# Performance work log

Hardware: AMD Instinct MI355X
Metric: run time of the kernel (lower is better)

The kernel has to match this reference:

```python
import jax, jax.numpy as jnp
import numpy as np

B, NO, NR, DIM, RNN = 64, 128, 512, 1024, 1000


def setup_inputs() -> dict:
    key = jax.random.key(0)
    ks = jax.random.split(key, 32)
    def rn(k, shape, s=0.02):
        return jax.random.normal(k, shape, dtype=jnp.float32) * s
    inp = {}
    inp['obj_labels'] = jax.random.randint(ks[0], (B, NO, 1), 0, 26)
    inp['obj_masks'] = jnp.ones((B, NO), jnp.float32)
    inp['rela_masks'] = jnp.ones((B, NR), jnp.float32)
    inp['rela_edges'] = jax.random.randint(ks[1], (B, NR, 2), 0, NO)
    inp['rela_feats'] = jax.random.normal(ks[2], (B, NR, 8), dtype=jnp.float32)
    inp['box_feats'] = jax.random.normal(ks[3], (B, NO, 5), dtype=jnp.float32)
    # parameters
    inp['emb_table'] = jax.random.uniform(ks[4], (26, 128), jnp.float32, -0.1, 0.1)
    inp['w_objfeat'] = rn(ks[5], (5, 128));        inp['b_objfeat'] = jnp.zeros((128,), jnp.float32)
    inp['w_cat'] = rn(ks[6], (256, 128));          inp['b_cat'] = jnp.zeros((128,), jnp.float32)
    inp['w_obj'] = rn(ks[7], (128, RNN));          inp['b_obj'] = jnp.zeros((RNN,), jnp.float32)
    inp['w_rela'] = rn(ks[8], (8, RNN));           inp['b_rela'] = jnp.zeros((RNN,), jnp.float32)
    inp['w_gnn'] = rn(ks[9], (3 * RNN, RNN));      inp['b_gnn'] = jnp.zeros((RNN,), jnp.float32)
    inp['w_att_obj'] = rn(ks[10], (RNN, 1));       inp['b_att_obj'] = jnp.zeros((1,), jnp.float32)
    inp['w_att_rela'] = rn(ks[11], (RNN, 1));      inp['b_att_rela'] = jnp.zeros((1,), jnp.float32)
    inp['w_read'] = rn(ks[12], (2 * RNN, DIM));    inp['b_read'] = jnp.zeros((DIM,), jnp.float32)
    inp['w_fc'] = rn(ks[13], (DIM, 32 * 14 * 6));  inp['b_fc'] = jnp.zeros((32 * 14 * 6,), jnp.float32)
    inp['wt1'] = rn(ks[14], (32, 25, 3, 3));       inp['bt1'] = jnp.zeros((25,), jnp.float32)
    inp['wt2'] = rn(ks[15], (25, 25, 3, 3));       inp['bt2'] = jnp.zeros((25,), jnp.float32)
    inp['wt3'] = rn(ks[16], (25, 25, 3, 3));       inp['bt3'] = jnp.zeros((25,), jnp.float32)
    inp['wt4'] = rn(ks[17], (25, 25, 3, 3));       inp['bt4'] = jnp.zeros((25,), jnp.float32)
    return inp


def _attn(feats, mask, w, b):
    # feats: (B, N, RNN); mask: (B, N)
    dot = (jnp.tanh(feats) @ w + b)[..., 0]              # (B, N)
    wgt = jax.nn.softmax(dot, axis=1) * mask
    wgt = wgt / jnp.sum(wgt, axis=1, keepdims=True)
    return jnp.einsum('bn,bnd->bd', wgt, feats)          # (B, RNN)


def _up2(x):
    return jnp.repeat(jnp.repeat(x, 2, axis=2), 2, axis=3)


def _convT(x, w, b):
    # torch ConvTranspose2d (stride=1, pad=0) == full-padded corr with flipped kernel
    k = jnp.transpose(w, (1, 0, 2, 3))[:, :, ::-1, ::-1]  # (out, in, 3, 3)
    y = jax.lax.conv_general_dilated(x, k, (1, 1), [(2, 2), (2, 2)],
                                     dimension_numbers=('NCHW', 'OIHW', 'NCHW'))
    return y + b[None, :, None, None]


def reference(obj_labels, obj_masks, rela_masks, rela_edges, rela_feats, box_feats,
              emb_table, w_objfeat, b_objfeat, w_cat, b_cat, w_obj, b_obj,
              w_rela, b_rela, w_gnn, b_gnn, w_att_obj, b_att_obj,
              w_att_rela, b_att_rela, w_read, b_read, w_fc, b_fc,
              wt1, bt1, wt2, bt2, wt3, bt3, wt4, bt4):
    relu = jax.nn.relu
    # embeddings (dropout = identity at inference)
    obj_embed = relu(emb_table[obj_labels])[:, :, 0, :]                   # (B, NO, 128)
    obj_f = relu(box_feats @ w_objfeat + b_objfeat)                       # (B, NO, 128)
    obj_embed = relu(jnp.concatenate([obj_f, obj_embed], -1) @ w_cat + b_cat)
    obj_vecs = relu(obj_embed @ w_obj + b_obj)                            # (B, NO, 1000)
    rela_vecs = relu(rela_feats @ w_rela + b_rela)                        # (B, NR, 1000)
    # GNN: gather endpoints, concat, linear+relu, mask
    s = jnp.take_along_axis(obj_vecs, rela_edges[:, :, 0:1], axis=1)      # (B, NR, 1000)
    o = jnp.take_along_axis(obj_vecs, rela_edges[:, :, 1:2], axis=1)
    t = jnp.concatenate([s, rela_vecs, o], axis=-1)                       # (B, NR, 3000)
    new_rela = relu(t @ w_gnn + b_gnn) * rela_masks[..., None]
    # attention pooling
    a_obj = _attn(obj_vecs, obj_masks, w_att_obj, b_att_obj)
    a_rel = _attn(new_rela, rela_masks, w_att_rela, b_att_rela)
    enc = relu(jnp.concatenate([a_obj, a_rel], axis=1) @ w_read + b_read)  # (B, DIM)
    # decoder
    x = (enc @ w_fc + b_fc).reshape(-1, 32, 14, 6)
    x = relu(_convT(_up2(x), wt1, bt1))
    x = relu(_convT(_up2(x), wt2, bt2))
    x = relu(_convT(_up2(x), wt3, bt3))
    x = relu(_convT(_up2(x), wt4, bt4))
    x = jax.nn.sigmoid(x)                                                  # (B, 25, 254, 126)
    return enc, x
```

## Files before the change

### kernel.cpp

```cpp
#include <hip/hip_runtime.h>
#include <hip/hip_bf16.h>
#include <hip/hip_fp16.h>

#define B_    64
#define NO_   128
#define NR_   512
#define RNN_  1000
#define DIM_  1024

typedef short short8 __attribute__((ext_vector_type(8)));
typedef float f32x4  __attribute__((ext_vector_type(4)));
typedef float f32x2v __attribute__((ext_vector_type(2)));
typedef float f32x4v __attribute__((ext_vector_type(4)));

static __device__ __forceinline__ float bf2f(unsigned short u) {
    union { unsigned int i; float f; } x; x.i = ((unsigned int)u) << 16; return x.f;
}
static __device__ __forceinline__ short f2bf_s(float f) {
    __hip_bfloat16 h = __float2bfloat16(f);
    return *reinterpret_cast<short*>(&h);
}

#define GLOAD_LDS16(gp, lp) \
    __builtin_amdgcn_global_load_lds((const __attribute__((address_space(1))) void*)(gp), \
                                     (__attribute__((address_space(3))) void*)(lp), 16, 0, 0)

__global__ void k_obj_embed(const int* __restrict__ labels,
                            const float* __restrict__ box_feats,
                            const float* __restrict__ emb_table,
                            const float* __restrict__ w_objfeat, const float* __restrict__ b_objfeat,
                            const float* __restrict__ w_cat, const float* __restrict__ b_cat,
                            __hip_bfloat16* __restrict__ out)
{
    const int row = blockIdx.x;
    const int tid = threadIdx.x;
    __shared__ __align__(16) float cat[256];
    __shared__ float bf[5];
    if (tid < 5) bf[tid] = box_feats[row * 5 + tid];
    __syncthreads();
    float acc = b_objfeat[tid];
#pragma unroll
    for (int k = 0; k < 5; ++k) acc += bf[k] * w_objfeat[k * 128 + tid];
    cat[tid] = fmaxf(acc, 0.f);
    const int label = labels[row];
    cat[128 + tid] = fmaxf(emb_table[label * 128 + tid], 0.f);
    __syncthreads();
    float acc2 = b_cat[tid];
#pragma unroll 4
    for (int k4 = 0; k4 < 64; ++k4) {
        const f32x4 c4 = *(const f32x4*)&cat[k4 * 4];
        acc2 += c4[0] * w_cat[(k4 * 4 + 0) * 128 + tid];
        acc2 += c4[1] * w_cat[(k4 * 4 + 1) * 128 + tid];
        acc2 += c4[2] * w_cat[(k4 * 4 + 2) * 128 + tid];
        acc2 += c4[3] * w_cat[(k4 * 4 + 3) * 128 + tid];
    }
    out[(size_t)row * 128 + tid] = __float2bfloat16(fmaxf(acc2, 0.f));
}

__global__ void k_transpose(const float* __restrict__ W, __hip_bfloat16* __restrict__ Wt,
                            int K, int N, int ldn, int Kpad)
{
    __shared__ float t[32][33];
    const int k0 = blockIdx.x * 32, n0 = blockIdx.y * 32;
    const int c = threadIdx.x & 31, r8 = threadIdx.x >> 5;
#pragma unroll
    for (int rr = r8; rr < 32; rr += 8) {
        int k = k0 + rr, n = n0 + c;
        t[rr][c] = (k < K && n < N) ? W[(size_t)k * ldn + n] : 0.f;
    }
    __syncthreads();
#pragma unroll
    for (int rr = r8; rr < 32; rr += 8)
        Wt[(size_t)(n0 + rr) * Kpad + k0 + c] = __float2bfloat16(t[c][rr]);
}

__global__ void k_weff(const float* __restrict__ w, float* __restrict__ wg, int IC, int OC)
{
    const int idx = blockIdx.x * 256 + threadIdx.x;
    if (idx >= IC * OC) return;
    const float* wp = w + (size_t)idx * 9;
    float wl[9];
#pragma unroll
    for (int k = 0; k < 9; ++k) wl[k] = wp[k];
    const float rm_[2][2][3] = {{{0.f,1.f,1.f},{1.f,0.f,0.f}},
                                {{0.f,0.f,1.f},{1.f,1.f,0.f}}};
    float* o = wg + (size_t)idx * 16;
#pragma unroll
    for (int py = 0; py < 2; ++py)
#pragma unroll
    for (int px = 0; px < 2; ++px)
#pragma unroll
    for (int r = 0; r < 2; ++r)
#pragma unroll
    for (int c = 0; c < 2; ++c) {
        float s = 0.f;
#pragma unroll
        for (int ky = 0; ky < 3; ++ky)
#pragma unroll
        for (int kx = 0; kx < 3; ++kx)
            s += rm_[py][r][ky] * rm_[px][c][kx] * wl[ky * 3 + kx];
        o[(r * 2 + c) * 4 + (py * 2 + px)] = s;
    }
}

__global__ void k_zero_border(float* __restrict__ buf, int PH, int PW, int IR0, int IR1, int IC0, int IC1)
{
    float* plane = buf + (size_t)blockIdx.x * PH * PW;
    const int tid = threadIdx.x;
    const int topN = IR0 * PW;
    for (int i = tid; i < topN; i += 256) plane[i] = 0.f;
    const int botBase = IR1 * PW, botN = (PH - IR1) * PW;
    for (int i = tid; i < botN; i += 256) plane[botBase + i] = 0.f;
    const int rows = IR1 - IR0;
    const int wL = IC0, wR = PW - IC1, wLR = wL + wR;
    const int n = rows * wLR;
    for (int i = tid; i < n; i += 256) {
        const int r = i / wLR, c = i - r * wLR;
        const int col = (c < wL) ? c : (IC1 + c - wL);
        plane[(IR0 + r) * PW + col] = 0.f;
    }
}

__global__ void k_rv(const float* __restrict__ rela_feats, const float* __restrict__ w_rela,
                     const float* __restrict__ b_rela, __hip_bfloat16* __restrict__ rv)
{
    const int tid = threadIdx.x;
    const int r0 = blockIdx.x * 16;
    __shared__ float rf[16][8];
    if (tid < 128) rf[tid >> 3][tid & 7] = rela_feats[(size_t)(r0 + (tid >> 3)) * 8 + (tid & 7)];
    __syncthreads();
    const int row = r0 + (tid >> 4);
    const int cg = (tid & 15) * 64;
    float rloc[8];
#pragma unroll
    for (int f = 0; f < 8; ++f) rloc[f] = rf[tid >> 4][f];
    __hip_bfloat16* orow = rv + (size_t)row * 1024;
#pragma unroll
    for (int ch = 0; ch < 8; ++ch) {
        const int c = cg + ch * 8;
        float a[8];
        if (c < RNN_) {
            const float4 b0 = *(const float4*)(b_rela + c);
            const float4 b1 = *(const float4*)(b_rela + c + 4);
            a[0] = b0.x; a[1] = b0.y; a[2] = b0.z; a[3] = b0.w;
            a[4] = b1.x; a[5] = b1.y; a[6] = b1.z; a[7] = b1.w;
#pragma unroll
            for (int f = 0; f < 8; ++f) {
                const float4 w0 = *(const float4*)(w_rela + f * RNN_ + c);
                const float4 w1 = *(const float4*)(w_rela + f * RNN_ + c + 4);
                const float rfv = rloc[f];
                a[0] += rfv * w0.x; a[1] += rfv * w0.y; a[2] += rfv * w0.z; a[3] += rfv * w0.w;
                a[4] += rfv * w1.x; a[5] += rfv * w1.y; a[6] += rfv * w1.z; a[7] += rfv * w1.w;
            }
#pragma unroll
            for (int j = 0; j < 8; ++j) a[j] = fmaxf(a[j], 0.f);
        } else {
#pragma unroll
            for (int j = 0; j < 8; ++j) a[j] = 0.f;
        }
        short8 pk;
#pragma unroll
        for (int j = 0; j < 8; ++j) pk[j] = f2bf_s(a[j]);
        *(short8*)(orow + c) = pk;
    }
}

template<int MODE>
__global__ __launch_bounds__(256)
void mfma_gemm(const __hip_bfloat16* __restrict__ A, const __hip_bfloat16* __restrict__ Bt, int Kpad,
               const float* __restrict__ bias, int ldc, int ncols,
               __hip_bfloat16* __restrict__ outB,
               const __half* __restrict__ P13H, const int* __restrict__ edges,
               const float* __restrict__ masks)
{
    __shared__ __align__(16) ushort smem[8704];
    ushort* lA = smem;
    ushort* lB = smem + 4096;
    const int tid = threadIdx.x;
    const int l = (blockIdx.x & 7) * ((int)gridDim.x >> 3) + ((int)blockIdx.x >> 3);
    const int n0 = (l & 7) * 128;
    const int m0 = (l >> 3) * 128;
    const int wave = tid >> 6, lane = tid & 63;
    const int wr = wave >> 1, wc = wave & 1;
    const int lr = lane >> 4, lc = lane & 15;
    const int lrow = lane >> 2;
    const int lcol = (lane & 3) * 8;
    f32x4 acc[4][4];
#pragma unroll
    for (int i = 0; i < 4; ++i)
#pragma unroll
        for (int j = 0; j < 4; ++j) acc[i][j] = (f32x4){0.f, 0.f, 0.f, 0.f};

    for (int k0 = 0; k0 < Kpad; k0 += 32) {
        __syncthreads();
#pragma unroll
        for (int j = 0; j < 2; ++j) {
            const int rbase = j * 64 + wave * 16;
            GLOAD_LDS16(A  + (size_t)(m0 + rbase + lrow) * Kpad + k0 + lcol, &lA[rbase * 32]);
            GLOAD_LDS16(Bt + (size_t)(n0 + rbase + lrow) * Kpad + k0 + lcol, &lB[rbase * 32]);
        }
        __syncthreads();
        short8 af[4], bfr[4];
#pragma unroll
        for (int mi = 0; mi < 4; ++mi)
            af[mi] = *(const short8*)&lA[(wr * 64 + mi * 16 + lc) * 32 + lr * 8];
#pragma unroll
        for (int ni = 0; ni < 4; ++ni)
            bfr[ni] = *(const short8*)&lB[(wc * 64 + ni * 16 + lc) * 32 + lr * 8];
#pragma unroll
        for (int mi = 0; mi < 4; ++mi)
#pragma unroll
            for (int ni = 0; ni < 4; ++ni)
                acc[mi][ni] = __builtin_amdgcn_mfma_f32_16x16x32_bf16(af[mi], bfr[ni], acc[mi][ni], 0, 0, 0);
    }

    float* ftile = (float*)smem;
    const int erow = tid >> 3;
    const int ecol0 = (tid & 7) * 16;
#pragma unroll
    for (int mi = 0; mi < 4; ++mi) {
        __syncthreads();
#pragma unroll
        for (int ni = 0; ni < 4; ++ni) {
            const int colL = wc * 64 + ni * 16 + lc;
#pragma unroll
            for (int r = 0; r < 4; ++r)
                ftile[(wr * 16 + lr * 4 + r) * 136 + colL] = acc[mi][ni][r];
        }
        __syncthreads();
        const int rowL = (erow < 16) ? (mi * 16 + erow) : (64 + mi * 16 + (erow - 16));
        const int grow = m0 + rowL;
        const int gcol = n0 + ecol0;
        float v[16];
#pragma unroll
        for (int j = 0; j < 4; ++j) {
            const f32x4 t4 = *(const f32x4*)&ftile[erow * 136 + ecol0 + j * 4];
            v[j*4+0] = t4[0]; v[j*4+1] = t4[1]; v[j*4+2] = t4[2]; v[j*4+3] = t4[3];
        }
        if (MODE == 0) {
            short8 pk0, pk1;
#pragma unroll
            for (int j = 0; j < 16; ++j) {
                const int c = gcol + j;
                const float bb = (c < ncols) ? bias[c] : 0.f;
                const short s = f2bf_s(fmaxf(v[j] + bb, 0.f));
                if (j < 8) pk0[j] = s; else pk1[j - 8] = s;
            }
            *(short8*)(outB + (size_t)grow * 1024 + gcol)     = pk0;
            *(short8*)(outB + (size_t)grow * 1024 + gcol + 8) = pk1;
        } else if (MODE == 1) {
            __half* outH = (__half*)outB;
            if (gcol + 15 < ncols) {
                __half h[16];
#pragma unroll
                for (int j = 0; j < 16; ++j) h[j] = __float2half(v[j]);
                *(short8*)(outH + (size_t)grow * ldc + gcol)     = *(short8*)&h[0];
                *(short8*)(outH + (size_t)grow * ldc + gcol + 8) = *(short8*)&h[8];
            } else {
#pragma unroll
                for (int j = 0; j < 16; ++j) {
                    const int c = gcol + j;
                    if (c < ncols) outH[(size_t)grow * ldc + c] = __float2half(v[j]);
                }
            }
        } else {
            const int b = grow >> 9;
            const int e0 = edges[grow * 2], e1 = edges[grow * 2 + 1];
            const float mk = masks[grow];
            const __half* p0 = P13H + (size_t)(b * NO_ + e0) * 2000 + gcol;
            const __half* p1 = P13H + (size_t)(b * NO_ + e1) * 2000 + RNN_ + gcol;
            if (gcol + 15 < ncols) {
                __half h0[16], h1[16];
                *(short8*)&h0[0] = *(const short8*)p0;  *(short8*)&h0[8] = *(const short8*)(p0 + 8);
                *(short8*)&h1[0] = *(const short8*)p1;  *(short8*)&h1[8] = *(const short8*)(p1 + 8);
                float bb[16];
#pragma unroll
                for (int j = 0; j < 4; ++j) {
                    const float4 b4 = *(const float4*)(bias + gcol + j * 4);
                    bb[j*4+0] = b4.x; bb[j*4+1] = b4.y; bb[j*4+2] = b4.z; bb[j*4+3] = b4.w;
                }
                short8 pk0, pk1;
#pragma unroll
                for (int j = 0; j < 16; ++j) {
                    float val = v[j] + bb[j] + __half2float(h0[j]) + __half2float(h1[j]);
                    const short s = f2bf_s(fmaxf(val, 0.f) * mk);
                    if (j < 8) pk0[j] = s; else pk1[j - 8] = s;
                }
                *(short8*)(outB + (size_t)grow * RNN_ + gcol)     = pk0;
                *(short8*)(outB + (size_t)grow * RNN_ + gcol + 8) = pk1;
            } else if (gcol < ncols) {
#pragma unroll
                for (int j = 0; j < 16; ++j) {
                    const int c = gcol + j;
                    if (c < ncols) {
                        float val = v[j] + bias[c] + __half2float(p0[j]) + __half2float(p1[j]);
                        outB[(size_t)grow * RNN_ + c] = __float2bfloat16(fmaxf(val, 0.f) * mk);
                    }
                }
            }
        }
    }
}

__global__ void k_gemm_sk(const float* __restrict__ A, const float* __restrict__ W,
                          float* __restrict__ part, int N, int K, int ldw, int Kc)
{
    __shared__ float As[16][68];
    __shared__ float Ws[16][68];
    const int tid = threadIdx.x;
    const int n0 = blockIdx.x * 64;
    const int kz = blockIdx.y;
    const int kstart = kz * Kc;
    const int kend = (kstart + Kc < K) ? (kstart + Kc) : K;
    const int ty = tid >> 4, tx = tid & 15;
    float acc[4][4] = {};
    for (int k0 = kstart; k0 < kend; k0 += 16) {
#pragma unroll
        for (int i = 0; i < 4; ++i) {
            int lin = i * 256 + tid;
            int r = lin >> 4, kk = lin & 15;
            int k = k0 + kk;
            As[kk][r] = (k < kend) ? A[(size_t)r * K + k] : 0.f;
            int kr = lin >> 6, c = lin & 63;
            int kw = k0 + kr, cc = n0 + c;
            Ws[kr][c] = (kw < kend && cc < N) ? W[(size_t)kw * ldw + cc] : 0.f;
        }
        __syncthreads();
#pragma unroll
        for (int kk = 0; kk < 16; ++kk) {
            const float4 av = *reinterpret_cast<const float4*>(&As[kk][ty * 4]);
            const float4 wv = *reinterpret_cast<const float4*>(&Ws[kk][tx * 4]);
            const float a4[4] = {av.x, av.y, av.z, av.w};
            const float w4[4] = {wv.x, wv.y, wv.z, wv.w};
#pragma unroll
            for (int i = 0; i < 4; ++i)
#pragma unroll
                for (int j = 0; j < 4; ++j) acc[i][j] += a4[i] * w4[j];
        }
        __syncthreads();
    }
#pragma unroll
    for (int i = 0; i < 4; ++i) {
        const int row = ty * 4 + i;
#pragma unroll
        for (int j = 0; j < 4; ++j) {
            const int col = n0 + tx * 4 + j;
            if (col < N)
                part[((size_t)kz * 64 + row) * N + col] = acc[i][j];
        }
    }
}

__global__ void k_sk_reduce(const float* __restrict__ part, const float* __restrict__ bias,
                            float* __restrict__ out, int N, int KS, int ldo, int act)
{
    const int idx = blockIdx.x * 256 + threadIdx.x;
    if (idx >= 64 * N) return;
    const int row = idx / N, col = idx - row * N;
    float s = bias[col];
    for (int z = 0; z < KS; ++z) s += part[((size_t)z * 64 + row) * N + col];
    if (act) s = fmaxf(s, 0.f);
    out[(size_t)row * ldo + col] = s;
}

__global__ void k_att_dot(const __hip_bfloat16* __restrict__ feats, const float* __restrict__ w_att,
                          const float* __restrict__ b_att, float* __restrict__ dot, int D, int ld)
{
    const int row = blockIdx.x;
    const int tid = threadIdx.x;
    const int c = tid * 4;
    float s = 0.f;
    if (c < D) {
        const ushort4 v = *(const ushort4*)(feats + (size_t)row * ld + c);
        const float4 wv = *(const float4*)(w_att + c);
        s  = tanhf(bf2f(v.x)) * wv.x;
        s += tanhf(bf2f(v.y)) * wv.y;
        s += tanhf(bf2f(v.z)) * wv.z;
        s += tanhf(bf2f(v.w)) * wv.w;
    }
#pragma unroll
    for (int o = 32; o > 0; o >>= 1) s += __shfl_down(s, o, 64);
    __shared__ float part[4];
    if ((tid & 63) == 0) part[tid >> 6] = s;
    __syncthreads();
    if (tid == 0) dot[row] = part[0] + part[1] + part[2] + part[3] + b_att[0];
}

__global__ void k_softmax(const float* __restrict__ dot, const float* __restrict__ mask,
                          float* __restrict__ wgt, int Nn)
{
    const int b = blockIdx.x, tid = threadIdx.x;
    __shared__ float red[512];
    float v = dot[b * Nn + tid];
    red[tid] = v; __syncthreads();
    for (int s = Nn >> 1; s > 0; s >>= 1) { if (tid < s) red[tid] = fmaxf(red[tid], red[tid + s]); __syncthreads(); }
    float mx = red[0]; __syncthreads();
    float e = expf(v - mx);
    red[tid] = e; __syncthreads();
    for (int s = Nn >> 1; s > 0; s >>= 1) { if (tid < s) red[tid] += red[tid + s]; __syncthreads(); }
    float sm = red[0]; __syncthreads();
    float w0 = (e / sm) * mask[b * Nn + tid];
    red[tid] = w0; __syncthreads();
    for (int s = Nn >> 1; s > 0; s >>= 1) { if (tid < s) red[tid] += red[tid + s]; __syncthreads(); }
    wgt[b * Nn + tid] = w0 / red[0];
}

__global__ void k_wsum(const __hip_bfloat16* __restrict__ feats, const float* __restrict__ wgt,
                       float* __restrict__ out, int Nn, int D, int ld, int ldo, int off)
{
    const int b = blockIdx.x;
    const int tid = threadIdx.x;
    __shared__ float wl[512];
    for (int i = tid; i < Nn; i += 256) wl[i] = wgt[b * Nn + i];
    __syncthreads();
    const int d0 = tid * 4;
    if (d0 >= D) return;
    float a0 = 0.f, a1 = 0.f, a2 = 0.f, a3 = 0.f;
    const __hip_bfloat16* fp = feats + (size_t)b * Nn * ld + d0;
#pragma unroll 8
    for (int n = 0; n < Nn; ++n) {
        const ushort4 v = *(const ushort4*)(fp + (size_t)n * ld);
        const float w = wl[n];
        a0 += w * bf2f(v.x); a1 += w * bf2f(v.y);
        a2 += w * bf2f(v.z); a3 += w * bf2f(v.w);
    }
    *(float4*)(out + (size_t)b * ldo + off + d0) = make_float4(a0, a1, a2, a3);
}

__global__ void k_convt5(const float* __restrict__ src, const float* __restrict__ wg,
                         const float* __restrict__ bias, float* __restrict__ dst,
                         int IC, int OC, int SH, int SW, int act,
                         int dro, int dco, int DPH, int DPW)
{
    const int QH = SH + 1, QW = SW + 1;
    const int ocg = blockIdx.y, b = blockIdx.z;
    const int tid = threadIdx.x;
    const int p = blockIdx.x * blockDim.x + tid;
    if (p >= QH * QW) return;
    const int a = p / QW, g = p % QW;
    const bool rm = (a > 0), rp = (a < SH);
    const bool cm = (g > 0), cp = (g < SW);
    f32x2v acc2[5][2];
#pragma unroll
    for (int ol = 0; ol < 5; ++ol) { acc2[ol][0] = (f32x2v){0.f, 0.f}; acc2[ol][1] = (f32x2v){0.f, 0.f}; }
    const float* sb = src + (size_t)(b * IC) * SH * SW;
    const int base = (a - 1) * SW + (g - 1);
    for (int ic = 0; ic < IC; ++ic) {
        const float* s = sb + (size_t)ic * SH * SW;
        const float s00 = (rm && cm) ? s[base] : 0.f;
        const float s01 = (rm && cp) ? s[base + 1] : 0.f;
        const float s10 = (rp && cm) ? s[base + SW] : 0.f;
        const float s11 = (rp && cp) ? s[base + SW + 1] : 0.f;
        const f32x2v b0 = {s00, s00}, b1 = {s01, s01}, b2 = {s10, s10}, b3 = {s11, s11};
        const float* wf = wg + ((size_t)ic * OC + ocg * 5) * 16;
#pragma unroll
        for (int ol = 0; ol < 5; ++ol) {
            const f32x4v w0 = *(const f32x4v*)(wf + ol * 16 + 0);
            const f32x4v w1 = *(const f32x4v*)(wf + ol * 16 + 4);
            const f32x4v w2 = *(const f32x4v*)(wf + ol * 16 + 8);
            const f32x4v w3 = *(const f32x4v*)(wf + ol * 16 + 12);
            acc2[ol][0] += b0 * __builtin_shufflevector(w0, w0, 0, 1);
            acc2[ol][0] += b1 * __builtin_shufflevector(w1, w1, 0, 1);
            acc2[ol][0] += b2 * __builtin_shufflevector(w2, w2, 0, 1);
            acc2[ol][0] += b3 * __builtin_shufflevector(w3, w3, 0, 1);
            acc2[ol][1] += b0 * __builtin_shufflevector(w0, w0, 2, 3);
            acc2[ol][1] += b1 * __builtin_shufflevector(w1, w1, 2, 3);
            acc2[ol][1] += b2 * __builtin_shufflevector(w2, w2, 2, 3);
            acc2[ol][1] += b3 * __builtin_shufflevector(w3, w3, 2, 3);
        }
    }
#pragma unroll
    for (int ol = 0; ol < 5; ++ol) {
        const int oc = ocg * 5 + ol;
        const float bv = bias[oc];
        float a00 = acc2[ol][0].x + bv, a01 = acc2[ol][0].y + bv;
        float a10 = acc2[ol][1].x + bv, a11 = acc2[ol][1].y + bv;
        if (act == 1) {
            a00 = fmaxf(a00, 0.f); a01 = fmaxf(a01, 0.f);
            a10 = fmaxf(a10, 0.f); a11 = fmaxf(a11, 0.f);
        } else {
            a00 = 1.f / (1.f + expf(-a00)); a01 = 1.f / (1.f + expf(-a01));
            a10 = 1.f / (1.f + expf(-a10)); a11 = 1.f / (1.f + expf(-a11));
        }
        float* dp = dst + ((size_t)(b * OC + oc) * DPH + 2 * a + dro) * DPW + 2 * g + dco;
        *reinterpret_cast<float2*>(dp)       = make_float2(a00, a01);
        *reinterpret_cast<float2*>(dp + DPW) = make_float2(a10, a11);
    }
}

__global__ void k_convtv(const float* __restrict__ src, int SPP, int SPW,
                         const float* __restrict__ wg,
                         const float* __restrict__ bias, float* __restrict__ dst,
                         int IC, int OC, int QH, int QW, int act, int LG,
                         int dro, int dco, int DPH, int DPW)
{
    const int ocg = blockIdx.y, b = blockIdx.z;
    const int tid = threadIdx.x;
    const int g = tid & ((1 << LG) - 1);
    const int a0 = blockIdx.x * ((256 >> LG) * 2) + (tid >> LG) * 2;
    if (g >= QW || a0 >= QH) return;
    f32x2v acc2[5][2][2];
#pragma unroll
    for (int ol = 0; ol < 5; ++ol)
#pragma unroll
        for (int q = 0; q < 2; ++q) { acc2[ol][q][0] = (f32x2v){0.f, 0.f}; acc2[ol][q][1] = (f32x2v){0.f, 0.f}; }
    const float* sb = src + (size_t)(b * IC) * SPP;
    const int rbase = a0 * SPW + g + 1;
    for (int ic = 0; ic < IC; ++ic) {
        const float* s = sb + (size_t)ic * SPP;
        f32x2v bc[3][2];
#pragma unroll
        for (int i = 0; i < 3; ++i) {
            const float v0 = s[rbase + i * SPW];
            const float v1 = s[rbase + i * SPW + 1];
            bc[i][0] = (f32x2v){v0, v0};
            bc[i][1] = (f32x2v){v1, v1};
        }
        const float* wf = wg + ((size_t)ic * OC + ocg * 5) * 16;
#pragma unroll
        for (int ol = 0; ol < 5; ++ol) {
            const f32x4v w0 = *(const f32x4v*)(wf + ol * 16 + 0);
            const f32x4v w1 = *(const f32x4v*)(wf + ol * 16 + 4);
            const f32x4v w2 = *(const f32x4v*)(wf + ol * 16 + 8);
            const f32x4v w3 = *(const f32x4v*)(wf + ol * 16 + 12);
            const f32x2v w0l = __builtin_shufflevector(w0, w0, 0, 1), w0h = __builtin_shufflevector(w0, w0, 2, 3);
            const f32x2v w1l = __builtin_shufflevector(w1, w1, 0, 1), w1h = __builtin_shufflevector(w1, w1, 2, 3);
            const f32x2v w2l = __builtin_shufflevector(w2, w2, 0, 1), w2h = __builtin_shufflevector(w2, w2, 2, 3);
            const f32x2v w3l = __builtin_shufflevector(w3, w3, 0, 1), w3h = __builtin_shufflevector(w3, w3, 2, 3);
#pragma unroll
            for (int q = 0; q < 2; ++q) {
                acc2[ol][q][0] += bc[q][0] * w0l;
                acc2[ol][q][0] += bc[q][1] * w1l;
                acc2[ol][q][0] += bc[q + 1][0] * w2l;
                acc2[ol][q][0] += bc[q + 1][1] * w3l;
                acc2[ol][q][1] += bc[q][0] * w0h;
                acc2[ol][q][1] += bc[q][1] * w1h;
                acc2[ol][q][1] += bc[q + 1][0] * w2h;
                acc2[ol][q][1] += bc[q + 1][1] * w3h;
            }
        }
    }
    const bool q1ok = (a0 + 1 < QH);
#pragma unroll
    for (int ol = 0; ol < 5; ++ol) {
        const int oc = ocg * 5 + ol;
        const float bv = bias[oc];
        float* dp0 = dst + ((size_t)(b * OC + oc) * DPH + 2 * a0 + dro) * DPW + 2 * g + dco;
#pragma unroll
        for (int q = 0; q < 2; ++q) {
            if (q == 1 && !q1ok) continue;
            float v0 = acc2[ol][q][0].x + bv, v1 = acc2[ol][q][0].y + bv;
            float v2 = acc2[ol][q][1].x + bv, v3 = acc2[ol][q][1].y + bv;
            if (act == 1) {
                v0 = fmaxf(v0, 0.f); v1 = fmaxf(v1, 0.f);
                v2 = fmaxf(v2, 0.f); v3 = fmaxf(v3, 0.f);
            } else {
                v0 = 1.f / (1.f + expf(-v0)); v1 = 1.f / (1.f + expf(-v1));
                v2 = 1.f / (1.f + expf(-v2)); v3 = 1.f / (1.f + expf(-v3));
            }
            float* dp = dp0 + q * 2 * DPW;
            *reinterpret_cast<float2*>(dp)       = make_float2(v0, v1);
            *reinterpret_cast<float2*>(dp + DPW) = make_float2(v2, v3);
        }
    }
}

extern "C" void kernel_launch(void* const* d_in, const int* in_sizes, int n_in,
                              void* d_out, int out_size, void* d_ws, size_t ws_size,
                              hipStream_t stream)
{
    const int*   obj_labels = (const int*)  d_in[0];
    const float* obj_masks  = (const float*)d_in[1];
    const float* rela_masks = (const float*)d_in[2];
    const int*   rela_edges = (const int*)  d_in[3];
    const float* rela_feats = (const float*)d_in[4];
    const float* box_feats  = (const float*)d_in[5];
    const float* emb_table  = (const float*)d_in[6];
    const float* w_objfeat  = (const float*)d_in[7];
    const float* b_objfeat  = (const float*)d_in[8];
    const float* w_cat      = (const float*)d_in[9];
    const float* b_cat      = (const float*)d_in[10];
    const float* w_obj      = (const float*)d_in[11];
    const float* b_obj      = (const float*)d_in[12];
    const float* w_rela     = (const float*)d_in[13];
    const float* b_rela     = (const float*)d_in[14];
    const float* w_gnn      = (const float*)d_in[15];
    const float* b_gnn      = (const float*)d_in[16];
    const float* w_att_obj  = (const float*)d_in[17];
    const float* b_att_obj  = (const float*)d_in[18];
    const float* w_att_rela = (const float*)d_in[19];
    const float* b_att_rela = (const float*)d_in[20];
    const float* w_read     = (const float*)d_in[21];
    const float* b_read     = (const float*)d_in[22];
    const float* w_fc       = (const float*)d_in[23];
    const float* b_fc       = (const float*)d_in[24];
    const float* wt1 = (const float*)d_in[25]; const float* bt1 = (const float*)d_in[26];
    const float* wt2 = (const float*)d_in[27]; const float* bt2 = (const float*)d_in[28];
    const float* wt3 = (const float*)d_in[29]; const float* bt3 = (const float*)d_in[30];
    const float* wt4 = (const float*)d_in[31]; const float* bt4 = (const float*)d_in[32];

    float* ws = (float*)d_ws;
    __hip_bfloat16* objembB  = (__hip_bfloat16*)(ws);
    __hip_bfloat16* obj_vecsB= (__hip_bfloat16*)(ws + 524288);
    __hip_bfloat16* w_objT   = (__hip_bfloat16*)(ws + 4718592);
    __hip_bfloat16* w1T      = (__hip_bfloat16*)(ws + 4784128);
    __hip_bfloat16* w2T      = (__hip_bfloat16*)(ws + 5308416);
    __hip_bfloat16* w3T      = (__hip_bfloat16*)(ws + 5832704);
    __half*         P13H     = (__half*)(ws + 6356992);
    __hip_bfloat16* rvB      = (__hip_bfloat16*)(ws + 14548992);
    __hip_bfloat16* newRB    = (__hip_bfloat16*)(ws + 31326208);
    float* dot_obj = ws + 47710208;
    float* dot_rel = dot_obj + 8192;
    float* wgt_obj = dot_rel + 32768;
    float* wgt_rel = wgt_obj + 8192;
    float* a_cat   = wgt_rel + 32768;
    float* part_enc = a_cat + 128000;
    float* part_fc  = part_enc + 524288;
    float* weff1 = ws + 49820672;
    float* weff2 = weff1 + 12800;
    float* weff3 = weff2 + 10000;
    float* weff4 = weff3 + 10000;
    float* d0  = ws;
    float* d1  = ws + 6356992;
    float* d2p = ws + 7028992;
    float* d3p = ws + 10619392;
    float* enc  = (float*)d_out;
    float* xout = (float*)d_out + 65536;

    k_transpose<<<dim3(4, 32),  256, 0, stream>>>(w_obj, w_objT, 128, RNN_, RNN_, 128);
    k_transpose<<<dim3(32, 32), 256, 0, stream>>>(w_gnn,                      w1T, RNN_, RNN_, RNN_, 1024);
    k_transpose<<<dim3(32, 32), 256, 0, stream>>>(w_gnn + (size_t)RNN_*RNN_,  w2T, RNN_, RNN_, RNN_, 1024);
    k_transpose<<<dim3(32, 32), 256, 0, stream>>>(w_gnn + (size_t)2*RNN_*RNN_,w3T, RNN_, RNN_, RNN_, 1024);
    k_weff<<<dim3(4), 256, 0, stream>>>(wt1, weff1, 32, 25);
    k_weff<<<dim3(3), 256, 0, stream>>>(wt2, weff2, 25, 25);
    k_weff<<<dim3(3), 256, 0, stream>>>(wt3, weff3, 25, 25);
    k_weff<<<dim3(3), 256, 0, stream>>>(wt4, weff4, 25, 25);
    k_obj_embed<<<dim3(8192), dim3(128), 0, stream>>>(obj_labels, box_feats, emb_table,
                                                      w_objfeat, b_objfeat, w_cat, b_cat, objembB);
    mfma_gemm<0><<<dim3(512), 256, 0, stream>>>(objembB, w_objT, 128, b_obj,
                                                0, RNN_, obj_vecsB, nullptr, nullptr, nullptr);
    mfma_gemm<1><<<dim3(512), 256, 0, stream>>>(obj_vecsB, w1T, 1024, nullptr,
                                                2000, RNN_, (__hip_bfloat16*)P13H, nullptr, nullptr, nullptr);
    mfma_gemm<1><<<dim3(512), 256, 0, stream>>>(obj_vecsB, w3T, 1024, nullptr,
                                                2000, RNN_, (__hip_bfloat16*)(P13H + RNN_), nullptr, nullptr, nullptr);
    k_rv<<<dim3(2048), 256, 0, stream>>>(rela_feats, w_rela, b_rela, rvB);
    mfma_gemm<2><<<dim3(2048), 256, 0, stream>>>(rvB, w2T, 1024, b_gnn,
                                                 0, RNN_, newRB, P13H, rela_edges, rela_masks);
    k_att_dot<<<8192,  256, 0, stream>>>(obj_vecsB, w_att_obj,  b_att_obj,  dot_obj, RNN_, 1024);
    k_att_dot<<<32768, 256, 0, stream>>>(newRB,     w_att_rela, b_att_rela, dot_rel, RNN_, RNN_);
    k_softmax<<<64, 128, 0, stream>>>(dot_obj, obj_masks,  wgt_obj, 128);
    k_softmax<<<64, 512, 0, stream>>>(dot_rel, rela_masks, wgt_rel, 512);
    k_wsum<<<dim3(64), 256, 0, stream>>>(obj_vecsB, wgt_obj, a_cat, 128, RNN_, 1024, 2000, 0);
    k_wsum<<<dim3(64), 256, 0, stream>>>(newRB,     wgt_rel, a_cat, 512, RNN_, RNN_, 2000, RNN_);
    k_gemm_sk<<<dim3(16, 8), 256, 0, stream>>>(a_cat, w_read, part_enc, DIM_, 2000, DIM_, 256);
    k_sk_reduce<<<dim3(256), 256, 0, stream>>>(part_enc, b_read, enc, DIM_, 8, DIM_, 1);
    k_gemm_sk<<<dim3(42, 8), 256, 0, stream>>>(enc, w_fc, part_fc, 2688, DIM_, 2688, 128);
    k_sk_reduce<<<dim3(672), 256, 0, stream>>>(part_fc, b_fc, d0, 2688, 8, 2688, 0);
    k_zero_border<<<dim3(1600), 256, 0, stream>>>(d2p, 66, 34, 1, 63, 2, 32);
    k_zero_border<<<dim3(1600), 256, 0, stream>>>(d3p, 130, 66, 1, 127, 2, 64);
    k_convt5<<<dim3(1, 5, 64), 256, 0, stream>>>(d0, weff1, bt1, d1, 32, 25, 14, 6, 1, 0, 0, 30, 14);
    k_convt5<<<dim3(2, 5, 64), 256, 0, stream>>>(d1, weff2, bt2, d2p, 25, 25, 30, 14, 1, 1, 2, 66, 34);
    k_convtv<<<dim3(4, 5, 64), 256, 0, stream>>>(d2p, 66 * 34, 34, weff3, bt3, d3p,
                                                 25, 25, 63, 31, 1, 5, 1, 2, 130, 66);
    k_convtv<<<dim3(16, 5, 64), 256, 0, stream>>>(d3p, 130 * 66, 66, weff4, bt4, xout,
                                                  25, 25, 127, 63, 2, 6, 0, 0, 254, 126);
}
```

Before: 784.5 us.

## Merge P1/P3 GEMMs into one wide launch and double GEMM K-step to 64

The two object-side projection GEMMs (w1 and w3 parts of w_gnn) are merged into one GEMM by placing w1T and w3T next to each other, giving a 2048-column output with padded stride 2048. The consumer in the gather epilogue is updated to match. The mfma_gemm main loop now loads 64 K elements per barrier pair into two LDS halves, halving the number of syncs per tile. The cost is double the LDS per block (32KB), which may reduce occupancy, and the padded P13 buffer is slightly larger.

```diff
diff --git a/kernel.cpp b/kernel.cpp
--- a/kernel.cpp
+++ b/kernel.cpp
@@ -171,15 +171,17 @@
                const float* __restrict__ bias, int ldc, int ncols,
                __hip_bfloat16* __restrict__ outB,
                const __half* __restrict__ P13H, const int* __restrict__ edges,
-               const float* __restrict__ masks)
-{
-    __shared__ __align__(16) ushort smem[8704];
-    ushort* lA = smem;
-    ushort* lB = smem + 4096;
+               const float* __restrict__ masks, int lgNT)
+{
+    __shared__ __align__(16) ushort smem[16384];
+    ushort* lA0 = smem;
+    ushort* lA1 = smem + 4096;
+    ushort* lB0 = smem + 8192;
+    ushort* lB1 = smem + 12288;
     const int tid = threadIdx.x;
     const int l = (blockIdx.x & 7) * ((int)gridDim.x >> 3) + ((int)blockIdx.x >> 3);
-    const int n0 = (l & 7) * 128;
-    const int m0 = (l >> 3) * 128;
+    const int n0 = (l & ((1 << lgNT) - 1)) * 128;
+    const int m0 = (l >> lgNT) * 128;
     const int wave = tid >> 6, lane = tid & 63;
     const int wr = wave >> 1, wc = wave & 1;
     const int lr = lane >> 4, lc = lane & 15;
@@ -191,27 +193,34 @@
 #pragma unroll
         for (int j = 0; j < 4; ++j) acc[i][j] = (f32x4){0.f, 0.f, 0.f, 0.f};
 
-    for (int k0 = 0; k0 < Kpad; k0 += 32) {
+    for (int k0 = 0; k0 < Kpad; k0 += 64) {
         __syncthreads();
 #pragma unroll
         for (int j = 0; j < 2; ++j) {
             const int rbase = j * 64 + wave * 16;
-            GLOAD_LDS16(A  + (size_t)(m0 + rbase + lrow) * Kpad + k0 + lcol, &lA[rbase * 32]);
-            GLOAD_LDS16(Bt + (size_t)(n0 + rbase + lrow) * Kpad + k0 + lcol, &lB[rbase * 32]);
+            GLOAD_LDS16(A  + (size_t)(m0 + rbase + lrow) * Kpad + k0 + lcol,      &lA0[rbase * 32]);
+            GLOAD_LDS16(A  + (size_t)(m0 + rbase + lrow) * Kpad + k0 + 32 + lcol, &lA1[rbase * 32]);
+            GLOAD_LDS16(Bt + (size_t)(n0 + rbase + lrow) * Kpad + k0 + lcol,      &lB0[rbase * 32]);
+            GLOAD_LDS16(Bt + (size_t)(n0 + rbase + lrow) * Kpad + k0 + 32 + lcol, &lB1[rbase * 32]);
         }
         __syncthreads();
-        short8 af[4], bfr[4];
-#pragma unroll
-        for (int mi = 0; mi < 4; ++mi)
-            af[mi] = *(const short8*)&lA[(wr * 64 + mi * 16 + lc) * 32 + lr * 8];
-#pragma unroll
-        for (int ni = 0; ni < 4; ++ni)
-            bfr[ni] = *(const short8*)&lB[(wc * 64 + ni * 16 + lc) * 32 + lr * 8];
-#pragma unroll
-        for (int mi = 0; mi < 4; ++mi)
+#pragma unroll
+        for (int h = 0; h < 2; ++h) {
+            const ushort* hA = h ? lA1 : lA0;
+            const ushort* hB = h ? lB1 : lB0;
+            short8 af[4], bfr[4];
+#pragma unroll
+            for (int mi = 0; mi < 4; ++mi)
+                af[mi] = *(const short8*)&hA[(wr * 64 + mi * 16 + lc) * 32 + lr * 8];
 #pragma unroll
             for (int ni = 0; ni < 4; ++ni)
-                acc[mi][ni] = __builtin_amdgcn_mfma_f32_16x16x32_bf16(af[mi], bfr[ni], acc[mi][ni], 0, 0, 0);
+                bfr[ni] = *(const short8*)&hB[(wc * 64 + ni * 16 + lc) * 32 + lr * 8];
+#pragma unroll
+            for (int mi = 0; mi < 4; ++mi)
+#pragma unroll
+                for (int ni = 0; ni < 4; ++ni)
+                    acc[mi][ni] = __builtin_amdgcn_mfma_f32_16x16x32_bf16(af[mi], bfr[ni], acc[mi][ni], 0, 0, 0);
+        }
     }
 
     float* ftile = (float*)smem;
@@ -267,8 +276,8 @@
             const int b = grow >> 9;
             const int e0 = edges[grow * 2], e1 = edges[grow * 2 + 1];
             const float mk = masks[grow];
-            const __half* p0 = P13H + (size_t)(b * NO_ + e0) * 2000 + gcol;
-            const __half* p1 = P13H + (size_t)(b * NO_ + e1) * 2000 + RNN_ + gcol;
+            const __half* p0 = P13H + (size_t)(b * NO_ + e0) * 2048 + gcol;
+            const __half* p1 = P13H + (size_t)(b * NO_ + e1) * 2048 + 1024 + gcol;
             if (gcol + 15 < ncols) {
                 __half h0[16], h1[16];
                 *(short8*)&h0[0] = *(const short8*)p0;  *(short8*)&h0[8] = *(const short8*)(p0 + 8);
@@ -604,19 +613,19 @@
     __hip_bfloat16* obj_vecsB= (__hip_bfloat16*)(ws + 524288);
     __hip_bfloat16* w_objT   = (__hip_bfloat16*)(ws + 4718592);
     __hip_bfloat16* w1T      = (__hip_bfloat16*)(ws + 4784128);
-    __hip_bfloat16* w2T      = (__hip_bfloat16*)(ws + 5308416);
-    __hip_bfloat16* w3T      = (__hip_bfloat16*)(ws + 5832704);
+    __hip_bfloat16* w3T      = (__hip_bfloat16*)(ws + 5308416);
+    __hip_bfloat16* w2T      = (__hip_bfloat16*)(ws + 5832704);
     __half*         P13H     = (__half*)(ws + 6356992);
-    __hip_bfloat16* rvB      = (__hip_bfloat16*)(ws + 14548992);
-    __hip_bfloat16* newRB    = (__hip_bfloat16*)(ws + 31326208);
-    float* dot_obj = ws + 47710208;
+    __hip_bfloat16* rvB      = (__hip_bfloat16*)(ws + 14745600);
+    __hip_bfloat16* newRB    = (__hip_bfloat16*)(ws + 31522816);
+    float* dot_obj = ws + 47906816;
     float* dot_rel = dot_obj + 8192;
     float* wgt_obj = dot_rel + 32768;
     float* wgt_rel = wgt_obj + 8192;
     float* a_cat   = wgt_rel + 32768;
     float* part_enc = a_cat + 128000;
     float* part_fc  = part_enc + 524288;
-    float* weff1 = ws + 49820672;
+    float* weff1 = ws + 50017184;
     float* weff2 = weff1 + 12800;
     float* weff3 = weff2 + 10000;
     float* weff4 = weff3 + 10000;
@@ -629,8 +638,8 @@
 
     k_transpose<<<dim3(4, 32),  256, 0, stream>>>(w_obj, w_objT, 128, RNN_, RNN_, 128);
     k_transpose<<<dim3(32, 32), 256, 0, stream>>>(w_gnn,                      w1T, RNN_, RNN_, RNN_, 1024);
+    k_transpose<<<dim3(32, 32), 256, 0, stream>>>(w_gnn + (size_t)2*RNN_*RNN_,w3T, RNN_, RNN_, RNN_, 1024);
     k_transpose<<<dim3(32, 32), 256, 0, stream>>>(w_gnn + (size_t)RNN_*RNN_,  w2T, RNN_, RNN_, RNN_, 1024);
-    k_transpose<<<dim3(32, 32), 256, 0, stream>>>(w_gnn + (size_t)2*RNN_*RNN_,w3T, RNN_, RNN_, RNN_, 1024);
     k_weff<<<dim3(4), 256, 0, stream>>>(wt1, weff1, 32, 25);
     k_weff<<<dim3(3), 256, 0, stream>>>(wt2, weff2, 25, 25);
     k_weff<<<dim3(3), 256, 0, stream>>>(wt3, weff3, 25, 25);
@@ -638,14 +647,12 @@
     k_obj_embed<<<dim3(8192), dim3(128), 0, stream>>>(obj_labels, box_feats, emb_table,
                                                       w_objfeat, b_objfeat, w_cat, b_cat, objembB);
     mfma_gemm<0><<<dim3(512), 256, 0, stream>>>(objembB, w_objT, 128, b_obj,
-                                                0, RNN_, obj_vecsB, nullptr, nullptr, nullptr);
-    mfma_gemm<1><<<dim3(512), 256, 0, stream>>>(obj_vecsB, w1T, 1024, nullptr,
-                                                2000, RNN_, (__hip_bfloat16*)P13H, nullptr, nullptr, nullptr);
-    mfma_gemm<1><<<dim3(512), 256, 0, stream>>>(obj_vecsB, w3T, 1024, nullptr,
-                                                2000, RNN_, (__hip_bfloat16*)(P13H + RNN_), nullptr, nullptr, nullptr);
+                                                0, RNN_, obj_vecsB, nullptr, nullptr, nullptr, 3);
+    mfma_gemm<1><<<dim3(1024), 256, 0, stream>>>(obj_vecsB, w1T, 1024, nullptr,
+                                                 2048, 2048, (__hip_bfloat16*)P13H, nullptr, nullptr, nullptr, 4);
     k_rv<<<dim3(2048), 256, 0, stream>>>(rela_feats, w_rela, b_rela, rvB);
     mfma_gemm<2><<<dim3(2048), 256, 0, stream>>>(rvB, w2T, 1024, b_gnn,
-                                                 0, RNN_, newRB, P13H, rela_edges, rela_masks);
+                                                 0, RNN_, newRB, P13H, rela_edges, rela_masks, 3);
     k_att_dot<<<8192,  256, 0, stream>>>(obj_vecsB, w_att_obj,  b_att_obj,  dot_obj, RNN_, 1024);
     k_att_dot<<<32768, 256, 0, stream>>>(newRB,     w_att_rela, b_att_rela, dot_rel, RNN_, RNN_);
     k_softmax<<<64, 128, 0, stream>>>(dot_obj, obj_masks,  wgt_obj, 128);
```

Result: faster. 757.0 us (-3.5%).
